# Kernel optimization log

Hardware: AMD Instinct MI355X
Metric: run time of the kernel (lower is better)

## Reference

```python
import jax, jax.numpy as jnp
import numpy as np
from jax import lax

B, T, E, D, A, C, FILT = 32, 1600, 1024, 1024, 512, 10, 100
SCALING = 2.0


def setup_inputs() -> dict:
    key = jax.random.key(0)
    ks = jax.random.split(key, 14)
    enc_hs_pad = jax.random.normal(ks[0], (B, T, E), dtype=jnp.float32)
    # lengths in [T//2, T] so every row has valid positions
    enc_hs_len = jax.random.randint(ks[1], (B,), T // 2, T + 1, dtype=jnp.int32)
    dec_z = jax.random.normal(ks[2], (B, D), dtype=jnp.float32)
    # previous attention weights: uniform over valid frames, normalized
    valid = (jnp.arange(T)[None, :] < enc_hs_len[:, None]).astype(jnp.float32)
    raw = jax.random.uniform(ks[3], (B, T), dtype=jnp.float32) * valid
    att_prev = raw / jnp.sum(raw, axis=1, keepdims=True)
    att_h = 0.1 * jax.random.normal(ks[4], (B, A), dtype=jnp.float32)
    att_c = 0.1 * jax.random.normal(ks[5], (B, A), dtype=jnp.float32)
    W_enc = jax.random.normal(ks[6], (A, E), dtype=jnp.float32) / np.sqrt(E)
    b_enc = jax.random.normal(ks[7], (A,), dtype=jnp.float32) * 0.01
    W_dec = jax.random.normal(ks[8], (A, D), dtype=jnp.float32) / np.sqrt(D)
    conv_w = jax.random.normal(ks[9], (C, 1, 2 * FILT + 1), dtype=jnp.float32) / np.sqrt(2 * FILT + 1)
    W_ih = jax.random.normal(ks[10], (4 * A, C), dtype=jnp.float32) / np.sqrt(C)
    W_hh = jax.random.normal(ks[11], (4 * A, A), dtype=jnp.float32) / np.sqrt(A)
    W_g = jax.random.normal(ks[12], (A,), dtype=jnp.float32) / np.sqrt(A)
    b_g = jnp.zeros((1,), dtype=jnp.float32)
    return {"enc_hs_pad": enc_hs_pad, "enc_hs_len": enc_hs_len, "dec_z": dec_z,
            "att_prev": att_prev, "att_h": att_h, "att_c": att_c,
            "W_enc": W_enc, "b_enc": b_enc, "W_dec": W_dec, "conv_w": conv_w,
            "W_ih": W_ih, "W_hh": W_hh, "W_g": W_g, "b_g": b_g}


def reference(enc_hs_pad, enc_hs_len, dec_z, att_prev, att_h, att_c,
              W_enc, b_enc, W_dec, conv_w, W_ih, W_hh, W_g, b_g):
    t_len = enc_hs_pad.shape[1]
    filts = (conv_w.shape[-1] - 1) // 2

    # precompute encoder projection (B, T, A)
    pre_enc = jnp.einsum('bte,ae->bta', enc_hs_pad, W_enc) + b_enc

    # location conv on previous attention: (B,1,T) -> (B,C,T), relu, global max-pool over T
    att_conv = lax.conv_general_dilated(att_prev[:, None, :], conv_w,
                                        window_strides=(1,), padding=[(filts, filts)],
                                        dimension_numbers=('NCH', 'OIH', 'NCH'))
    att_feat = jnp.max(jax.nn.relu(att_conv), axis=-1)  # (B, C)

    # LSTMCell (no bias), pytorch gate order i, f, g, o
    gates = att_feat @ W_ih.T + att_h @ W_hh.T  # (B, 4A)
    i, f, g, o = jnp.split(gates, 4, axis=-1)
    c_new = jax.nn.sigmoid(f) * att_c + jax.nn.sigmoid(i) * jnp.tanh(g)
    h_new = jax.nn.sigmoid(o) * jnp.tanh(c_new)  # (B, A)

    dec_proj = dec_z @ W_dec.T  # (B, A)
    # scores (B, T)
    e = jnp.tanh(h_new[:, None, :] + pre_enc + dec_proj[:, None, :]) @ W_g + b_g

    mask = jnp.arange(t_len)[None, :] >= enc_hs_len[:, None]  # True = pad
    e = jnp.where(mask, jnp.finfo(e.dtype).min, e)
    w = jax.nn.softmax(SCALING * e, axis=1)  # (B, T)

    ctx = jnp.einsum('bt,bte->be', w, enc_hs_pad)  # (B, E)
    return ctx, w, h_new, c_new
```

## Files before the change

### kernel.cpp

```cpp
#include <hip/hip_runtime.h>
#include <hip/hip_bf16.h>

#define BB 32
#define TT 1600
#define EE 1024
#define AA 512
#define CC 10
#define KW 201

typedef __attribute__((ext_vector_type(8))) short short8;
typedef __attribute__((ext_vector_type(4))) float f32x4;

__device__ __forceinline__ float sigm(float x) { return 1.f / (1.f + expf(-x)); }

__device__ __forceinline__ unsigned int cvt2(float a, float b) {
    float2 f2; f2.x = a; f2.y = b;
    __hip_bfloat162 h = __float22bfloat162_rn(f2);
    unsigned int r;
    __builtin_memcpy(&r, &h, 4);
    return r;
}

__device__ __forceinline__ void gl_lds16(const void* g, void* l) {
    __builtin_amdgcn_global_load_lds(
        (const __attribute__((address_space(1))) unsigned int*)g,
        (__attribute__((address_space(3))) unsigned int*)l, 16, 0, 0);
}

#define AF_OFF   0
#define R_OFF    320
#define E_OFF    16704
#define WBF_OFF  67904

#define CTX_OFF 0
#define W_OFF   32768
#define H_OFF   83968
#define C_OFF   100352

__global__ void prep_kernel(const float* __restrict__ att_prev,
                            const float* __restrict__ conv_w,
                            const float* __restrict__ W_enc,
                            float* __restrict__ af,
                            unsigned short* __restrict__ Wbf,
                            float* __restrict__ out) {
    int bx = blockIdx.x, tid = threadIdx.x;
    if (bx >= 832) {
        int i = (bx - 832) * 256 + tid;
        reinterpret_cast<float4*>(out + CTX_OFF)[i] = (float4){0.f, 0.f, 0.f, 0.f};
        return;
    }
    if (bx >= 320) {
        int i = (bx - 320) * 256 + tid;
        float4 v = reinterpret_cast<const float4*>(W_enc)[i];
        uint2 p;
        p.x = cvt2(v.x, v.y);
        p.y = cvt2(v.z, v.w);
        reinterpret_cast<uint2*>(Wbf)[i] = p;
        return;
    }
    int b = bx / 10, c = bx % 10;
    __shared__ float xs[1808];
    __shared__ float wsm[KW];
    __shared__ float red[256];
    const float* xp = att_prev + b * TT;
    for (int i = tid; i < 1808; i += 256) {
        int g = i - 100;
        xs[i] = (g >= 0 && g < TT) ? xp[g] : 0.f;
    }
    if (tid < KW) wsm[tid] = conv_w[c * KW + tid];
    __syncthreads();
    float mx = 0.f;
    #pragma unroll 1
    for (int sweep = 0; sweep < 2; ++sweep) {
        int t0 = sweep * 1024 + tid * 4;
        if (t0 >= TT) break;
        float a0 = xs[t0], a1 = xs[t0 + 1], a2 = xs[t0 + 2], a3 = xs[t0 + 3];
        float s0 = 0.f, s1 = 0.f, s2 = 0.f, s3 = 0.f;
        #pragma unroll 4
        for (int k = 0; k < KW; ++k) {
            float w = wsm[k];
            s0 += w * a0; s1 += w * a1; s2 += w * a2; s3 += w * a3;
            a0 = a1; a1 = a2; a2 = a3;
            a3 = xs[t0 + k + 4];
        }
        mx = fmaxf(mx, fmaxf(fmaxf(s0, s1), fmaxf(s2, s3)));
    }
    red[tid] = mx; __syncthreads();
    for (int s = 128; s > 0; s >>= 1) {
        if (tid < s) red[tid] = fmaxf(red[tid], red[tid + s]);
        __syncthreads();
    }
    if (tid == 0) af[b * CC + c] = red[0];
}

__global__ void gates_lstm_kernel(const float* __restrict__ af,
                                  const float* __restrict__ att_h,
                                  const float* __restrict__ dec_z,
                                  const float* __restrict__ att_c,
                                  const float* __restrict__ W_ih,
                                  const float* __restrict__ W_hh,
                                  const float* __restrict__ W_dec,
                                  float* __restrict__ out,
                                  float* __restrict__ r_ws) {
    __shared__ float gsm[8][32];
    __shared__ float dsm[8][32];
    int tid = threadIdx.x;
    int a0 = blockIdx.x * 2;
    int b = tid & 31;
    if (tid < 256) {
        int u = tid >> 5;
        int gate = u >> 1, ai = u & 1;
        int j = gate * 512 + a0 + ai;
        float s = 0.f;
        #pragma unroll
        for (int k = 0; k < 10; ++k) s += af[b * 10 + k] * W_ih[j * 10 + k];
        const float4* wr = reinterpret_cast<const float4*>(W_hh + (size_t)j * 512);
        const float4* hr = reinterpret_cast<const float4*>(att_h + b * 512);
        #pragma unroll 4
        for (int k = 0; k < 128; ++k) {
            float4 w = wr[k], h = hr[k];
            s += w.x * h.x + w.y * h.y + w.z * h.z + w.w * h.w;
        }
        gsm[u][b] = s;
    } else {
        int v = (tid - 256) >> 5;
        int ai = v & 1, q = v >> 1;
        int a = a0 + ai;
        const float4* wr = reinterpret_cast<const float4*>(W_dec + (size_t)a * 1024) + q * 64;
        const float4* zr = reinterpret_cast<const float4*>(dec_z + (size_t)b * 1024) + q * 64;
        float s = 0.f;
        #pragma unroll 4
        for (int k = 0; k < 64; ++k) {
            float4 w = wr[k], z = zr[k];
            s += w.x * z.x + w.y * z.y + w.z * z.z + w.w * z.w;
        }
        dsm[v][b] = s;
    }
    __syncthreads();
    if (tid < 64) {
        int ai = tid >> 5;
        int a = a0 + ai;
        float ig = gsm[ai][b], fg = gsm[2 + ai][b], gg = gsm[4 + ai][b], og = gsm[6 + ai][b];
        float cn = sigm(fg) * att_c[b * 512 + a] + sigm(ig) * tanhf(gg);
        float hn = sigm(og) * tanhf(cn);
        out[H_OFF + b * 512 + a] = hn;
        out[C_OFF + b * 512 + a] = cn;
        float dec = dsm[ai][b] + dsm[2 + ai][b] + dsm[4 + ai][b] + dsm[6 + ai][b];
        r_ws[b * 512 + a] = hn + dec;
    }
}

__global__ void __launch_bounds__(512, 2)
score_gemm_kernel(const float* __restrict__ enc,
                  const unsigned short* __restrict__ Wbf,
                  const float* __restrict__ b_enc,
                  const float* __restrict__ r_ws,
                  const float* __restrict__ W_g,
                  float* __restrict__ e_ws) {
    __shared__ __align__(16) float As[512 * 4];
    __shared__ __align__(16) short Bs[2048 * 8];
    __shared__ float e_part[8][64];

    int tid = threadIdx.x;
    int lane = tid & 63, wv = tid >> 6;
    int col = lane & 15, quad = lane >> 4;
    int m0 = blockIdx.x * 64;

    {
    }
    int a_row = tid >> 3;
    int a_kg = (tid & 7) ^ (a_row & 7);
    const float* a_src = enc + (size_t)(m0 + a_row) * EE + a_kg * 4;
    const unsigned short* b_src[4];
    #pragma unroll
    for (int j = 0; j < 4; ++j) {
        int s = tid + 512 * j;
        int n = s >> 2;
        int kg = (s & 3) ^ ((n >> 1) & 3);
        b_src[j] = Wbf + (size_t)n * EE + kg * 8;
    }

    f32x4 acc[4][4];
    #pragma unroll
    for (int mt = 0; mt < 4; ++mt)
        #pragma unroll
        for (int nt = 0; nt < 4; ++nt)
            acc[mt][nt] = (f32x4){0.f, 0.f, 0.f, 0.f};

    int aswz = col & 7;
    int bswz = (col >> 1) & 3;

    for (int k0 = 0; k0 < EE; k0 += 32) {
        __syncthreads();
        gl_lds16(a_src + k0, &As[tid * 4]);
        #pragma unroll
        for (int j = 0; j < 4; ++j)
            gl_lds16(b_src[j] + k0, &Bs[(tid + 512 * j) * 8]);
        __syncthreads();

        short8 a_frag[4];
        #pragma unroll
        for (int mt = 0; mt < 4; ++mt) {
            int s0 = (mt * 16 + col) * 8 + ((2 * quad) ^ aswz);
            float4 fa = *reinterpret_cast<const float4*>(&As[s0 * 4]);
            float4 fb = *reinterpret_cast<const float4*>(&As[(s0 ^ 1) * 4]);
            uint4 u;
            u.x = cvt2(fa.x, fa.y); u.y = cvt2(fa.z, fa.w);
            u.z = cvt2(fb.x, fb.y); u.w = cvt2(fb.z, fb.w);
            __builtin_memcpy(&a_frag[mt], &u, 16);
        }
        #pragma unroll
        for (int nt = 0; nt < 4; ++nt) {
            int slot = (wv * 64 + nt * 16 + col) * 4 + (quad ^ bswz);
            short8 bf = *reinterpret_cast<const short8*>(&Bs[slot * 8]);
            #pragma unroll
            for (int mt = 0; mt < 4; ++mt)
                acc[mt][nt] = __builtin_amdgcn_mfma_f32_16x16x32_bf16(
                    a_frag[mt], bf, acc[mt][nt], 0, 0, 0);
        }
    }

    int bb = blockIdx.x / 25;
    float wg[4], bn[4], rr[4];
    #pragma unroll
    for (int nt = 0; nt < 4; ++nt) {
        int n = wv * 64 + nt * 16 + col;
        wg[nt] = W_g[n];
        bn[nt] = b_enc[n];
        rr[nt] = r_ws[bb * AA + n];
    }
    #pragma unroll
    for (int mt = 0; mt < 4; ++mt) {
        #pragma unroll
        for (int reg = 0; reg < 4; ++reg) {
            float p = 0.f;
            #pragma unroll
            for (int nt = 0; nt < 4; ++nt)
                p += wg[nt] * tanhf(acc[mt][nt][reg] + bn[nt] + rr[nt]);
            p += __shfl_xor(p, 1);
            p += __shfl_xor(p, 2);
            p += __shfl_xor(p, 4);
            p += __shfl_xor(p, 8);
            if (col == 0) e_part[wv][mt * 16 + quad * 4 + reg] = p;
        }
    }
    __syncthreads();
    if (tid < 64) {
        float s = 0.f;
        #pragma unroll
        for (int i = 0; i < 8; ++i) s += e_part[i][tid];
        e_ws[m0 + tid] = s;
    }
}

__global__ void softmax_kernel(const float* __restrict__ e_ws,
                               const int* __restrict__ lens,
                               float* __restrict__ w_out) {
    int b = blockIdx.x, tid = threadIdx.x;
    int len = lens[b];
    const float* e = e_ws + b * TT;
    __shared__ float red[256];
    float mx = -3.4e38f;
    for (int t = tid; t < len; t += 256) mx = fmaxf(mx, e[t]);
    red[tid] = mx; __syncthreads();
    for (int s = 128; s > 0; s >>= 1) {
        if (tid < s) red[tid] = fmaxf(red[tid], red[tid + s]);
        __syncthreads();
    }
    mx = red[0]; __syncthreads();
    float sum = 0.f;
    for (int t = tid; t < len; t += 256) sum += expf(2.f * (e[t] - mx));
    red[tid] = sum; __syncthreads();
    for (int s = 128; s > 0; s >>= 1) {
        if (tid < s) red[tid] += red[tid + s];
        __syncthreads();
    }
    float inv = 1.f / red[0];
    for (int t = tid; t < TT; t += 256)
        w_out[b * TT + t] = (t < len) ? expf(2.f * (e[t] - mx)) * inv : 0.f;
}

__global__ void ctx_kernel(const float* __restrict__ enc,
                           const float* __restrict__ w,
                           float* __restrict__ ctx) {
    int b = blockIdx.x, seg = blockIdx.y;
    int t0 = seg * 64;
    const float* wrow = w + b * TT + t0;
    const float* base = enc + ((size_t)(b * TT + t0)) * EE + threadIdx.x * 4;
    float4 acc = {0.f, 0.f, 0.f, 0.f};
    #pragma unroll 1
    for (int i = 0; i < 64; i += 4) {
        float w0 = wrow[i], w1 = wrow[i + 1], w2 = wrow[i + 2], w3 = wrow[i + 3];
        float4 v0 = *reinterpret_cast<const float4*>(base + (size_t)(i + 0) * EE);
        float4 v1 = *reinterpret_cast<const float4*>(base + (size_t)(i + 1) * EE);
        float4 v2 = *reinterpret_cast<const float4*>(base + (size_t)(i + 2) * EE);
        float4 v3 = *reinterpret_cast<const float4*>(base + (size_t)(i + 3) * EE);
        acc.x += w0 * v0.x + w1 * v1.x + w2 * v2.x + w3 * v3.x;
        acc.y += w0 * v0.y + w1 * v1.y + w2 * v2.y + w3 * v3.y;
        acc.z += w0 * v0.z + w1 * v1.z + w2 * v2.z + w3 * v3.z;
        acc.w += w0 * v0.w + w1 * v1.w + w2 * v2.w + w3 * v3.w;
    }
    float* dst = ctx + b * EE + threadIdx.x * 4;
    atomicAdd(dst + 0, acc.x);
    atomicAdd(dst + 1, acc.y);
    atomicAdd(dst + 2, acc.z);
    atomicAdd(dst + 3, acc.w);
}

extern "C" void kernel_launch(void* const* d_in, const int* in_sizes, int n_in,
                              void* d_out, int out_size, void* d_ws, size_t ws_size,
                              hipStream_t stream) {
    const float* enc      = (const float*)d_in[0];
    const int*   lens     = (const int*)d_in[1];
    const float* dec_z    = (const float*)d_in[2];
    const float* att_prev = (const float*)d_in[3];
    const float* att_h    = (const float*)d_in[4];
    const float* att_c    = (const float*)d_in[5];
    const float* W_enc    = (const float*)d_in[6];
    const float* b_enc    = (const float*)d_in[7];
    const float* W_dec    = (const float*)d_in[8];
    const float* conv_w   = (const float*)d_in[9];
    const float* W_ih     = (const float*)d_in[10];
    const float* W_hh     = (const float*)d_in[11];
    const float* W_g      = (const float*)d_in[12];

    float* out = (float*)d_out;
    float* ws  = (float*)d_ws;
    float* af   = ws + AF_OFF;
    float* r_ws = ws + R_OFF;
    float* e_ws = ws + E_OFF;
    unsigned short* Wbf = (unsigned short*)(ws + WBF_OFF);

    prep_kernel<<<864, 256, 0, stream>>>(att_prev, conv_w, W_enc, af, Wbf, out);
    gates_lstm_kernel<<<256, 512, 0, stream>>>(af, att_h, dec_z, att_c,
                                               W_ih, W_hh, W_dec, out, r_ws);
    score_gemm_kernel<<<800, 512, 0, stream>>>(enc, Wbf, b_enc, r_ws, W_g, e_ws);
    softmax_kernel<<<BB, 256, 0, stream>>>(e_ws, lens, out + W_OFF);
    ctx_kernel<<<dim3(BB, 25), 256, 0, stream>>>(enc, out + W_OFF, out + CTX_OFF);
}
```

Baseline: 532.4 us.

## Load GEMM fragments directly from global into registers with double buffering

Drops the LDS staging of encoder and weight tiles in the score GEMM. Each wave now loads its MFMA fragments straight from global memory into registers, using two register buffers so the next K-slice is fetched while the current one is computed. This removes the per-iteration __syncthreads barriers and LDS traffic. In exchange, the encoder A tile is read redundantly by all 8 waves and register pressure rises, so the launch bound no longer requests 2 blocks per CU.

```diff
diff --git a/kernel.cpp b/kernel.cpp
--- a/kernel.cpp
+++ b/kernel.cpp
@@ -19,12 +19,6 @@
     unsigned int r;
     __builtin_memcpy(&r, &h, 4);
     return r;
-}
-
-__device__ __forceinline__ void gl_lds16(const void* g, void* l) {
-    __builtin_amdgcn_global_load_lds(
-        (const __attribute__((address_space(1))) unsigned int*)g,
-        (__attribute__((address_space(3))) unsigned int*)l, 16, 0, 0);
 }
 
 #define AF_OFF   0
@@ -150,15 +144,13 @@
     }
 }
 
-__global__ void __launch_bounds__(512, 2)
+__global__ void __launch_bounds__(512)
 score_gemm_kernel(const float* __restrict__ enc,
                   const unsigned short* __restrict__ Wbf,
                   const float* __restrict__ b_enc,
                   const float* __restrict__ r_ws,
                   const float* __restrict__ W_g,
                   float* __restrict__ e_ws) {
-    __shared__ __align__(16) float As[512 * 4];
-    __shared__ __align__(16) short Bs[2048 * 8];
     __shared__ float e_part[8][64];
 
     int tid = threadIdx.x;
@@ -166,19 +158,14 @@
     int col = lane & 15, quad = lane >> 4;
     int m0 = blockIdx.x * 64;
 
-    {
-    }
-    int a_row = tid >> 3;
-    int a_kg = (tid & 7) ^ (a_row & 7);
-    const float* a_src = enc + (size_t)(m0 + a_row) * EE + a_kg * 4;
-    const unsigned short* b_src[4];
-    #pragma unroll
-    for (int j = 0; j < 4; ++j) {
-        int s = tid + 512 * j;
-        int n = s >> 2;
-        int kg = (s & 3) ^ ((n >> 1) & 3);
-        b_src[j] = Wbf + (size_t)n * EE + kg * 8;
-    }
+    const float* aptr[4];
+    const unsigned short* bptr[4];
+    #pragma unroll
+    for (int mt = 0; mt < 4; ++mt)
+        aptr[mt] = enc + (size_t)(m0 + mt * 16 + col) * EE + quad * 8;
+    #pragma unroll
+    for (int nt = 0; nt < 4; ++nt)
+        bptr[nt] = Wbf + (size_t)(wv * 64 + nt * 16 + col) * EE + quad * 8;
 
     f32x4 acc[4][4];
     #pragma unroll
@@ -187,37 +174,55 @@
         for (int nt = 0; nt < 4; ++nt)
             acc[mt][nt] = (f32x4){0.f, 0.f, 0.f, 0.f};
 
-    int aswz = col & 7;
-    int bswz = (col >> 1) & 3;
-
-    for (int k0 = 0; k0 < EE; k0 += 32) {
-        __syncthreads();
-        gl_lds16(a_src + k0, &As[tid * 4]);
-        #pragma unroll
-        for (int j = 0; j < 4; ++j)
-            gl_lds16(b_src[j] + k0, &Bs[(tid + 512 * j) * 8]);
-        __syncthreads();
-
-        short8 a_frag[4];
+    float4 xa0[4], xa1[4], ya0[4], ya1[4];
+    short8 xb[4], yb[4];
+
+    auto load_x = [&](int k) {
         #pragma unroll
         for (int mt = 0; mt < 4; ++mt) {
-            int s0 = (mt * 16 + col) * 8 + ((2 * quad) ^ aswz);
-            float4 fa = *reinterpret_cast<const float4*>(&As[s0 * 4]);
-            float4 fb = *reinterpret_cast<const float4*>(&As[(s0 ^ 1) * 4]);
+            xa0[mt] = *reinterpret_cast<const float4*>(aptr[mt] + k);
+            xa1[mt] = *reinterpret_cast<const float4*>(aptr[mt] + k + 4);
+        }
+        #pragma unroll
+        for (int nt = 0; nt < 4; ++nt)
+            xb[nt] = *reinterpret_cast<const short8*>(bptr[nt] + k);
+    };
+    auto load_y = [&](int k) {
+        #pragma unroll
+        for (int mt = 0; mt < 4; ++mt) {
+            ya0[mt] = *reinterpret_cast<const float4*>(aptr[mt] + k);
+            ya1[mt] = *reinterpret_cast<const float4*>(aptr[mt] + k + 4);
+        }
+        #pragma unroll
+        for (int nt = 0; nt < 4; ++nt)
+            yb[nt] = *reinterpret_cast<const short8*>(bptr[nt] + k);
+    };
+    auto comp = [&](float4* a0, float4* a1, short8* bb) {
+        short8 af[4];
+        #pragma unroll
+        for (int mt = 0; mt < 4; ++mt) {
             uint4 u;
-            u.x = cvt2(fa.x, fa.y); u.y = cvt2(fa.z, fa.w);
-            u.z = cvt2(fb.x, fb.y); u.w = cvt2(fb.z, fb.w);
-            __builtin_memcpy(&a_frag[mt], &u, 16);
-        }
-        #pragma unroll
-        for (int nt = 0; nt < 4; ++nt) {
-            int slot = (wv * 64 + nt * 16 + col) * 4 + (quad ^ bswz);
-            short8 bf = *reinterpret_cast<const short8*>(&Bs[slot * 8]);
+            u.x = cvt2(a0[mt].x, a0[mt].y);
+            u.y = cvt2(a0[mt].z, a0[mt].w);
+            u.z = cvt2(a1[mt].x, a1[mt].y);
+            u.w = cvt2(a1[mt].z, a1[mt].w);
+            __builtin_memcpy(&af[mt], &u, 16);
+        }
+        #pragma unroll
+        for (int nt = 0; nt < 4; ++nt)
             #pragma unroll
             for (int mt = 0; mt < 4; ++mt)
                 acc[mt][nt] = __builtin_amdgcn_mfma_f32_16x16x32_bf16(
-                    a_frag[mt], bf, acc[mt][nt], 0, 0, 0);
-        }
+                    af[mt], bb[nt], acc[mt][nt], 0, 0, 0);
+    };
+
+    load_x(0);
+    #pragma unroll 1
+    for (int k0 = 0; k0 < EE; k0 += 64) {
+        load_y(k0 + 32);
+        comp(xa0, xa1, xb);
+        if (k0 + 64 < EE) load_x(k0 + 64);
+        comp(ya0, ya1, yb);
     }
 
     int bb = blockIdx.x / 25;
```

After: 718.9 us. +35.0%, slower.
